# Kernel optimization log

Hardware: AMD Instinct MI355X
Metric: run time of the kernel (lower is better)

The kernel has to match this reference:

```python
import jax, jax.numpy as jnp
import numpy as np

_DN = ('NCHW', 'OIHW', 'NCHW')


def _gaussian_kernel1d(ksize, sigma):
    x = np.arange(ksize, dtype=np.float32) - ksize // 2
    g = np.exp(-x ** 2 / (2.0 * sigma ** 2))
    return (g / g.sum()).astype(np.float32)


def _nms_kernels():
    # kornia get_canny_nms_kernel: kernel k = center - neighbor at angle k*45deg (0deg = +x/right)
    k = np.zeros((8, 1, 3, 3), dtype=np.float32)
    offs = [(0, 1), (-1, 1), (-1, 0), (-1, -1), (0, -1), (1, -1), (1, 0), (1, 1)]
    for i, (dy, dx) in enumerate(offs):
        k[i, 0, 1, 1] = 1.0
        k[i, 0, 1 + dy, 1 + dx] = -1.0
    return k


def _conv(x, w, padding):
    return jax.lax.conv_general_dilated(x, w, (1, 1), padding, dimension_numbers=_DN)


def _canny_magnitude(data):
    eps = 1e-6
    x = (data + 1.0) / 2.0
    # rgb -> grayscale (kornia weights)
    rgb_w = jnp.array([0.299, 0.587, 0.114], dtype=x.dtype)
    gray = jnp.einsum('bchw,c->bhw', x, rgb_w)[:, None]  # [B,1,H,W]
    # gaussian blur 5x5, sigma=1, reflect border (kornia default), separable
    g1d = jnp.asarray(_gaussian_kernel1d(5, 1.0), dtype=x.dtype)
    p = jnp.pad(gray, ((0, 0), (0, 0), (2, 2), (2, 2)), mode='reflect')
    blurred = _conv(_conv(p, g1d.reshape(1, 1, 1, 5), 'VALID'), g1d.reshape(1, 1, 5, 1), 'VALID')
    # sobel spatial gradient (normalized=False), replicate padding
    sob_x = jnp.array([[-1., 0., 1.], [-2., 0., 2.], [-1., 0., 1.]], dtype=x.dtype)
    sob = jnp.stack([sob_x, sob_x.T])[:, None]  # [2,1,3,3]
    bp = jnp.pad(blurred, ((0, 0), (0, 0), (1, 1), (1, 1)), mode='edge')
    grads = _conv(bp, sob, 'VALID')  # [B,2,H,W]
    gx, gy = grads[:, 0:1], grads[:, 1:2]
    magnitude = jnp.sqrt(gx * gx + gy * gy + eps)  # [B,1,H,W]
    # angle rounded to nearest 45 degrees
    ang45 = jnp.round(jnp.rad2deg(jnp.arctan2(gy, gx)) / 45.0)
    # non-maximum suppression: center-minus-neighbor along 8 directions (zero pad)
    nms_k = jnp.asarray(_nms_kernels(), dtype=x.dtype)
    nms_mag = _conv(magnitude, nms_k, ((1, 1), (1, 1)))  # [B,8,H,W]
    idx_pos = ang45.astype(jnp.int32) % 8
    idx_neg = (idx_pos + 4) % 8
    sel_pos = jnp.take_along_axis(nms_mag, idx_pos, axis=1)
    sel_neg = jnp.take_along_axis(nms_mag, idx_neg, axis=1)
    is_max = jnp.minimum(sel_pos, sel_neg) > 0.0
    return magnitude * is_max


def setup_inputs() -> dict:
    key = jax.random.key(0)
    data = jax.random.normal(key, (16, 3, 512, 512), dtype=jnp.float32)
    return {'data': data}


def reference(data):
    # EdgeOperator.forward: canny((data+1)/2)[0] -> NMS'd gradient magnitude [B,1,H,W]
    return _canny_magnitude(data)
```

## Files before the change

kernel.cpp:

```cpp
#include <hip/hip_runtime.h>
#include <math.h>

#define IMH 512
#define IMW 512
#define RB    16
#define NBAND 32
#define NWC   10
#define OUTW  56

__device__ __forceinline__ int reflect_i(int v, int n) {
    if (v < 0) v = -v;
    if (v >= n) v = 2 * n - 2 - v;
    return v;
}
__device__ __forceinline__ float dpp_shr1(float x) {
    int i = __float_as_int(x);
    return __int_as_float(__builtin_amdgcn_update_dpp(i, i, 0x138, 0xF, 0xF, false));
}
__device__ __forceinline__ float dpp_shl1(float x) {
    int i = __float_as_int(x);
    return __int_as_float(__builtin_amdgcn_update_dpp(i, i, 0x130, 0xF, 0xF, false));
}

template <bool YB>
__device__ __forceinline__ void run_band(const float* __restrict__ p0,
                                         const float* __restrict__ p1,
                                         const float* __restrict__ p2,
                                         float* __restrict__ outp,
                                         int y0, int rx, int cx,
                                         int ixm, int ixp, int lane) {
    const float w0 = 0.05448868f, w1 = 0.24420134f, w2 = 0.40261995f;

    float h0 = 0, h1 = 0, h2 = 0, h3 = 0;
    float b_1 = 0, b_0 = 0, bl_1 = 0, bl_0 = 0, br_1 = 0, br_0 = 0;
    float m_1 = 0, m_0 = 0, ml_1 = 0, ml_0 = 0, mr_1 = 0, mr_0 = 0;
    float gxp = 0, gyp = 0;

    auto process = [&](int yL, float gray) {
        float gm1 = dpp_shr1(gray);
        float gm2 = dpp_shr1(gm1);
        float gp1 = dpp_shl1(gray);
        float gp2 = dpp_shl1(gp1);
        float hnew = w0 * (gm2 + gp2) + w1 * (gm1 + gp1) + w2 * gray;
        float bnew = w0 * (h0 + hnew) + w1 * (h1 + h3) + w2 * h2;
        float blnew = __shfl(bnew, ixm);
        float brnew = __shfl(bnew, ixp);
        int u = yL - 3;
        float ta  = (YB && u == 0) ? b_0 : b_1;
        float tla = (YB && u == 0) ? bl_0 : bl_1;
        float tra = (YB && u == 0) ? br_0 : br_1;
        float tb  = (YB && u == IMH - 1) ? b_0 : bnew;
        float tlb = (YB && u == IMH - 1) ? bl_0 : blnew;
        float trb = (YB && u == IMH - 1) ? br_0 : brnew;
        float gx = (tra - tla) + 2.0f * (br_0 - bl_0) + (trb - tlb);
        float gy = (tlb - tla) + 2.0f * (tb - ta) + (trb - tra);
        float mnew = sqrtf(gx * gx + gy * gy + 1e-6f);
        if ((unsigned)cx >= (unsigned)IMW) mnew = 0.0f;
        float mlnew = dpp_shr1(mnew);
        float mrnew = dpp_shl1(mnew);
        int s = yL - 4;
        if (s >= y0) {
            float pm  = (YB && s == 0) ? 0.0f : m_1;
            float pml = (YB && s == 0) ? 0.0f : ml_1;
            float pmr = (YB && s == 0) ? 0.0f : mr_1;
            float nm  = (YB && s == IMH - 1) ? 0.0f : mnew;
            float nml = (YB && s == IMH - 1) ? 0.0f : mlnew;
            float nmr = (YB && s == IMH - 1) ? 0.0f : mrnew;
            float ax = fabsf(gxp), ay = fabsf(gyp);
            bool ew = (ay <= 0.41421356237f * ax);
            bool ns = (ay >= 2.41421356237f * ax);
            bool d1 = (gxp * gyp > 0.0f);
            float n1 = ew ? mr_0 : (ns ? nm : (d1 ? pmr : nmr));
            float n2 = ew ? ml_0 : (ns ? pm : (d1 ? nml : pml));
            float mag = m_0;
            float o = (mag > n1 && mag > n2) ? mag : 0.0f;
            if (lane >= 4 && lane < 60 && (unsigned)cx < (unsigned)IMW)
                __builtin_nontemporal_store(o, &outp[(size_t)s * IMW + cx]);
        }
        h0 = h1; h1 = h2; h2 = h3; h3 = hnew;
        b_1 = b_0;  b_0 = bnew;
        bl_1 = bl_0; bl_0 = blnew;
        br_1 = br_0; br_0 = brnew;
        m_1 = m_0;  m_0 = mnew;
        ml_1 = ml_0; ml_0 = mlnew;
        mr_1 = mr_0; mr_0 = mrnew;
        gxp = gx; gyp = gy;
    };

    int ya = reflect_i(y0 - 4, IMH) * IMW;
    float rA = p0[ya + rx], gA = p1[ya + rx], cA = p2[ya + rx];
    int yb = reflect_i(y0 - 3, IMH) * IMW;
    float rB = p0[yb + rx], gB = p1[yb + rx], cB = p2[yb + rx];

    #pragma unroll 2
    for (int tt = 0; tt < (RB + 8) / 2; ++tt) {
        int yL = y0 - 4 + 2 * tt;
        float grayA = 0.1495f * rA + 0.2935f * gA + 0.057f * cA + 0.5f;
        int yr = reflect_i(yL + 2, IMH) * IMW;
        rA = p0[yr + rx]; gA = p1[yr + rx]; cA = p2[yr + rx];
        process(yL, grayA);
        float grayB = 0.1495f * rB + 0.2935f * gB + 0.057f * cB + 0.5f;
        int yr2 = reflect_i(yL + 3, IMH) * IMW;
        rB = p0[yr2 + rx]; gB = p1[yr2 + rx]; cB = p2[yr2 + rx];
        process(yL + 1, grayB);
    }
}

__global__ __launch_bounds__(256)
void canny_stream(const float* __restrict__ data, float* __restrict__ out) {
    const int lane = threadIdx.x & 63;
    const int wid  = (blockIdx.x << 2) + (threadIdx.x >> 6);
    const int wc   = wid % NWC;
    const int t2   = wid / NWC;
    const int band = t2 & (NBAND - 1);
    const int bat  = t2 >> 5;

    const int c0 = OUTW * wc - 4;
    const int cx = c0 + lane;
    const int y0 = band * RB;

    const size_t plane = (size_t)(IMH * IMW);
    const float* p0 = data + (size_t)bat * 3 * plane;
    const float* p1 = p0 + plane;
    const float* p2 = p1 + plane;
    float* outp = out + (size_t)bat * plane;

    const int rx  = reflect_i(cx, IMW);
    const int ixm = (cx - 1 < 0 ? 0 : (cx - 1 >= IMW ? IMW - 1 : cx - 1)) - c0;
    const int ixp = (cx + 1 < 0 ? 0 : (cx + 1 >= IMW ? IMW - 1 : cx + 1)) - c0;

    if (band == 0 || band == NBAND - 1)
        run_band<true>(p0, p1, p2, outp, y0, rx, cx, ixm, ixp, lane);
    else
        run_band<false>(p0, p1, p2, outp, y0, rx, cx, ixm, ixp, lane);
}

extern "C" void kernel_launch(void* const* d_in, const int* in_sizes, int n_in,
                              void* d_out, int out_size, void* d_ws, size_t ws_size,
                              hipStream_t stream) {
    const float* data = (const float*)d_in[0];
    float* out = (float*)d_out;
    int B = in_sizes[0] / (3 * IMH * IMW);
    int blocks = (B * NBAND * NWC) / 4;
    canny_stream<<<blocks, dim3(256, 1, 1), 0, stream>>>(data, out);
}
```

Baseline: 93.21 us.

## Process two columns per lane with float2 loads and x-border specialization

Each lane now handles two adjacent columns, so a wave covers 128 columns with a 4-column halo on each side instead of 64 with a 4-column halo. This cuts redundant halo loads and compute, and halves the number of waves (NWC 10→5). Loads and stores become float2/64-bit vectors, and the __shfl neighbour exchanges are replaced by DPP shifts. A new XB template splits border tiles from interior ones so interior tiles skip column reflection and validity checks. The cost is higher register pressure and fewer waves in flight, which lowers occupancy and latency hiding.

After: 98.03 us. 5.2% more time.

```diff
diff --git a/kernel.cpp b/kernel.cpp
--- a/kernel.cpp
+++ b/kernel.cpp
@@ -5,8 +5,8 @@
 #define IMW 512
 #define RB    16
 #define NBAND 32
-#define NWC   10
-#define OUTW  56
+#define NWC   5
+#define OUTW  120
 
 __device__ __forceinline__ int reflect_i(int v, int n) {
     if (v < 0) v = -v;
@@ -22,87 +22,133 @@
     return __int_as_float(__builtin_amdgcn_update_dpp(i, i, 0x130, 0xF, 0xF, false));
 }
 
-template <bool YB>
+template <bool YB, bool XB>
 __device__ __forceinline__ void run_band(const float* __restrict__ p0,
                                          const float* __restrict__ p1,
                                          const float* __restrict__ p2,
                                          float* __restrict__ outp,
-                                         int y0, int rx, int cx,
-                                         int ixm, int ixp, int lane) {
+                                         int y0, int c0, int lane) {
     const float w0 = 0.05448868f, w1 = 0.24420134f, w2 = 0.40261995f;
+    const int cx0 = c0 + 2 * lane, cx1 = cx0 + 1;
+    int rx0 = 0, rx1 = 0;
+    bool vx0 = true, vx1 = true;
+    if (XB) {
+        rx0 = reflect_i(cx0, IMW); rx1 = reflect_i(cx1, IMW);
+        vx0 = (unsigned)cx0 < (unsigned)IMW;
+        vx1 = (unsigned)cx1 < (unsigned)IMW;
+    }
+    const bool storeok = (lane >= 2) && (lane <= 61) &&
+                         (!XB || (unsigned)cx0 < (unsigned)IMW);
 
-    float h0 = 0, h1 = 0, h2 = 0, h3 = 0;
-    float b_1 = 0, b_0 = 0, bl_1 = 0, bl_0 = 0, br_1 = 0, br_0 = 0;
-    float m_1 = 0, m_0 = 0, ml_1 = 0, ml_0 = 0, mr_1 = 0, mr_0 = 0;
-    float gxp = 0, gyp = 0;
+    float hA0 = 0, hA1 = 0, hA2 = 0, hA3 = 0, hB0 = 0, hB1 = 0, hB2 = 0, hB3 = 0;
+    float bp0_1 = 0, bp1_1 = 0, bp0_0 = 0, bp1_0 = 0;
+    float bl_1 = 0, bl_0 = 0, br_1 = 0, br_0 = 0;
+    float mp0_1 = 0, mp1_1 = 0, mp0_0 = 0, mp1_0 = 0;
+    float ml_1 = 0, ml_0 = 0, mr_1 = 0, mr_0 = 0;
+    float gxp0 = 0, gxp1 = 0, gyp0 = 0, gyp1 = 0;
 
-    auto process = [&](int yL, float gray) {
-        float gm1 = dpp_shr1(gray);
-        float gm2 = dpp_shr1(gm1);
-        float gp1 = dpp_shl1(gray);
-        float gp2 = dpp_shl1(gp1);
-        float hnew = w0 * (gm2 + gp2) + w1 * (gm1 + gp1) + w2 * gray;
-        float bnew = w0 * (h0 + hnew) + w1 * (h1 + h3) + w2 * h2;
-        float blnew = __shfl(bnew, ixm);
-        float brnew = __shfl(bnew, ixp);
+    auto loadrow = [&](int y, float2& R, float2& G, float2& Bc) {
+        int yy = YB ? reflect_i(y, IMH) : y;
+        int yo = yy * IMW;
+        if (XB) {
+            R.x = p0[yo + rx0]; R.y = p0[yo + rx1];
+            G.x = p1[yo + rx0]; G.y = p1[yo + rx1];
+            Bc.x = p2[yo + rx0]; Bc.y = p2[yo + rx1];
+        } else {
+            R  = *(const float2*)(p0 + yo + cx0);
+            G  = *(const float2*)(p1 + yo + cx0);
+            Bc = *(const float2*)(p2 + yo + cx0);
+        }
+    };
+    auto grayf = [&](const float2& R, const float2& G, const float2& Bc) {
+        float2 g;
+        g.x = 0.1495f * R.x + 0.2935f * G.x + 0.057f * Bc.x;
+        g.y = 0.1495f * R.y + 0.2935f * G.y + 0.057f * Bc.y;
+        return g;
+    };
+
+    auto process = [&](int yL, float2 Gp) {
+        float g1L = dpp_shr1(Gp.y);
+        float g0L = dpp_shr1(Gp.x);
+        float g0R = dpp_shl1(Gp.x);
+        float g1R = dpp_shl1(Gp.y);
+        float h0n = w0 * (g0L + g0R) + w1 * (g1L + Gp.y) + w2 * Gp.x;
+        float h1n = w0 * (g1L + g1R) + w1 * (Gp.x + g0R) + w2 * Gp.y;
+        float b0n = w0 * (hA0 + h0n) + w1 * (hA1 + hA3) + w2 * hA2;
+        float b1n = w0 * (hB0 + h1n) + w1 * (hB1 + hB3) + w2 * hB2;
+        float bl1n = dpp_shr1(b1n);
+        float br0n = dpp_shl1(b0n);
+        if (XB) {
+            if (cx0 == 0)       bl1n = b0n;
+            if (cx1 == IMW - 1) br0n = b1n;
+        }
         int u = yL - 3;
-        float ta  = (YB && u == 0) ? b_0 : b_1;
-        float tla = (YB && u == 0) ? bl_0 : bl_1;
-        float tra = (YB && u == 0) ? br_0 : br_1;
-        float tb  = (YB && u == IMH - 1) ? b_0 : bnew;
-        float tlb = (YB && u == IMH - 1) ? bl_0 : blnew;
-        float trb = (YB && u == IMH - 1) ? br_0 : brnew;
-        float gx = (tra - tla) + 2.0f * (br_0 - bl_0) + (trb - tlb);
-        float gy = (tlb - tla) + 2.0f * (tb - ta) + (trb - tra);
-        float mnew = sqrtf(gx * gx + gy * gy + 1e-6f);
-        if ((unsigned)cx >= (unsigned)IMW) mnew = 0.0f;
-        float mlnew = dpp_shr1(mnew);
-        float mrnew = dpp_shl1(mnew);
+        float t_b0 = bp0_1, t_b1 = bp1_1, t_bl = bl_1, t_br = br_1;
+        float n_b0 = b0n,   n_b1 = b1n,   n_bl = bl1n, n_br = br0n;
+        if (YB) {
+            if (u == 0)       { t_b0 = bp0_0; t_b1 = bp1_0; t_bl = bl_0; t_br = br_0; }
+            if (u == IMH - 1) { n_b0 = bp0_0; n_b1 = bp1_0; n_bl = bl_0; n_br = br_0; }
+        }
+        float gx0 = (t_b1 - t_bl) + 2.0f * (bp1_0 - bl_0) + (n_b1 - n_bl);
+        float gy0 = (n_bl - t_bl) + 2.0f * (n_b0 - t_b0) + (n_b1 - t_b1);
+        float gx1 = (t_br - t_b0) + 2.0f * (br_0 - bp0_0) + (n_br - n_b0);
+        float gy1 = (n_b0 - t_b0) + 2.0f * (n_b1 - t_b1) + (n_br - t_br);
+        float mg0 = __builtin_amdgcn_sqrtf(gx0 * gx0 + gy0 * gy0 + 1e-6f);
+        float mg1 = __builtin_amdgcn_sqrtf(gx1 * gx1 + gy1 * gy1 + 1e-6f);
+        if (XB) { if (!vx0) mg0 = 0.0f; if (!vx1) mg1 = 0.0f; }
+        float mln = dpp_shr1(mg1);
+        float mrn = dpp_shl1(mg0);
         int s = yL - 4;
         if (s >= y0) {
-            float pm  = (YB && s == 0) ? 0.0f : m_1;
-            float pml = (YB && s == 0) ? 0.0f : ml_1;
-            float pmr = (YB && s == 0) ? 0.0f : mr_1;
-            float nm  = (YB && s == IMH - 1) ? 0.0f : mnew;
-            float nml = (YB && s == IMH - 1) ? 0.0f : mlnew;
-            float nmr = (YB && s == IMH - 1) ? 0.0f : mrnew;
-            float ax = fabsf(gxp), ay = fabsf(gyp);
-            bool ew = (ay <= 0.41421356237f * ax);
-            bool ns = (ay >= 2.41421356237f * ax);
-            bool d1 = (gxp * gyp > 0.0f);
-            float n1 = ew ? mr_0 : (ns ? nm : (d1 ? pmr : nmr));
-            float n2 = ew ? ml_0 : (ns ? pm : (d1 ? nml : pml));
-            float mag = m_0;
-            float o = (mag > n1 && mag > n2) ? mag : 0.0f;
-            if (lane >= 4 && lane < 60 && (unsigned)cx < (unsigned)IMW)
-                __builtin_nontemporal_store(o, &outp[(size_t)s * IMW + cx]);
+            float pm0 = mp0_1, pm1 = mp1_1, pml = ml_1, pmr = mr_1;
+            float nm0 = mg0,   nm1 = mg1,   nml = mln,  nmr = mrn;
+            if (YB) {
+                if (s == 0)       { pm0 = 0; pm1 = 0; pml = 0; pmr = 0; }
+                if (s == IMH - 1) { nm0 = 0; nm1 = 0; nml = 0; nmr = 0; }
+            }
+            float ax0 = fabsf(gxp0), ay0 = fabsf(gyp0);
+            bool ew0 = ay0 <= 0.41421356237f * ax0;
+            bool ns0 = ay0 >= 2.41421356237f * ax0;
+            bool d10 = gxp0 * gyp0 > 0.0f;
+            float n1a = ew0 ? mp1_0 : (ns0 ? nm0 : (d10 ? pm1 : nm1));
+            float n2a = ew0 ? ml_0  : (ns0 ? pm0 : (d10 ? nml : pml));
+            float o0 = (mp0_0 > n1a && mp0_0 > n2a) ? mp0_0 : 0.0f;
+            float ax1 = fabsf(gxp1), ay1 = fabsf(gyp1);
+            bool ew1 = ay1 <= 0.41421356237f * ax1;
+            bool ns1 = ay1 >= 2.41421356237f * ax1;
+            bool d11 = gxp1 * gyp1 > 0.0f;
+            float n1b = ew1 ? mr_0  : (ns1 ? nm1 : (d11 ? pmr : nmr));
+            float n2b = ew1 ? mp0_0 : (ns1 ? pm1 : (d11 ? nm0 : pm0));
+            float o1 = (mp1_0 > n1b && mp1_0 > n2b) ? mp1_0 : 0.0f;
+            if (storeok) {
+                union { float f[2]; unsigned long long u; } pk;
+                pk.f[0] = o0; pk.f[1] = o1;
+                __builtin_nontemporal_store(
+                    pk.u, (unsigned long long*)(outp + (size_t)s * IMW + cx0));
+            }
         }
-        h0 = h1; h1 = h2; h2 = h3; h3 = hnew;
-        b_1 = b_0;  b_0 = bnew;
-        bl_1 = bl_0; bl_0 = blnew;
-        br_1 = br_0; br_0 = brnew;
-        m_1 = m_0;  m_0 = mnew;
-        ml_1 = ml_0; ml_0 = mlnew;
-        mr_1 = mr_0; mr_0 = mrnew;
-        gxp = gx; gyp = gy;
+        hA0 = hA1; hA1 = hA2; hA2 = hA3; hA3 = h0n;
+        hB0 = hB1; hB1 = hB2; hB2 = hB3; hB3 = h1n;
+        bp0_1 = bp0_0; bp0_0 = b0n;  bp1_1 = bp1_0; bp1_0 = b1n;
+        bl_1 = bl_0; bl_0 = bl1n;    br_1 = br_0; br_0 = br0n;
+        mp0_1 = mp0_0; mp0_0 = mg0;  mp1_1 = mp1_0; mp1_0 = mg1;
+        ml_1 = ml_0; ml_0 = mln;     mr_1 = mr_0; mr_0 = mrn;
+        gxp0 = gx0; gxp1 = gx1; gyp0 = gy0; gyp1 = gy1;
     };
 
-    int ya = reflect_i(y0 - 4, IMH) * IMW;
-    float rA = p0[ya + rx], gA = p1[ya + rx], cA = p2[ya + rx];
-    int yb = reflect_i(y0 - 3, IMH) * IMW;
-    float rB = p0[yb + rx], gB = p1[yb + rx], cB = p2[yb + rx];
+    float2 rA, gA, cA, rB, gB, cB;
+    loadrow(y0 - 4, rA, gA, cA);
+    loadrow(y0 - 3, rB, gB, cB);
 
     #pragma unroll 2
     for (int tt = 0; tt < (RB + 8) / 2; ++tt) {
         int yL = y0 - 4 + 2 * tt;
-        float grayA = 0.1495f * rA + 0.2935f * gA + 0.057f * cA + 0.5f;
-        int yr = reflect_i(yL + 2, IMH) * IMW;
-        rA = p0[yr + rx]; gA = p1[yr + rx]; cA = p2[yr + rx];
-        process(yL, grayA);
-        float grayB = 0.1495f * rB + 0.2935f * gB + 0.057f * cB + 0.5f;
-        int yr2 = reflect_i(yL + 3, IMH) * IMW;
-        rB = p0[yr2 + rx]; gB = p1[yr2 + rx]; cB = p2[yr2 + rx];
-        process(yL + 1, grayB);
+        float2 GA = grayf(rA, gA, cA);
+        loadrow(yL + 2, rA, gA, cA);
+        process(yL, GA);
+        float2 GB = grayf(rB, gB, cB);
+        loadrow(yL + 3, rB, gB, cB);
+        process(yL + 1, GB);
     }
 }
 
@@ -116,7 +162,6 @@
     const int bat  = t2 >> 5;
 
     const int c0 = OUTW * wc - 4;
-    const int cx = c0 + lane;
     const int y0 = band * RB;
 
     const size_t plane = (size_t)(IMH * IMW);
@@ -125,14 +170,15 @@
     const float* p2 = p1 + plane;
     float* outp = out + (size_t)bat * plane;
 
-    const int rx  = reflect_i(cx, IMW);
-    const int ixm = (cx - 1 < 0 ? 0 : (cx - 1 >= IMW ? IMW - 1 : cx - 1)) - c0;
-    const int ixp = (cx + 1 < 0 ? 0 : (cx + 1 >= IMW ? IMW - 1 : cx + 1)) - c0;
-
-    if (band == 0 || band == NBAND - 1)
-        run_band<true>(p0, p1, p2, outp, y0, rx, cx, ixm, ixp, lane);
-    else
-        run_band<false>(p0, p1, p2, outp, y0, rx, cx, ixm, ixp, lane);
+    const bool yb = (band == 0) || (band == NBAND - 1);
+    const bool xb = (wc == 0) || (wc == NWC - 1);
+    if (yb) {
+        if (xb) run_band<true, true >(p0, p1, p2, outp, y0, c0, lane);
+        else    run_band<true, false>(p0, p1, p2, outp, y0, c0, lane);
+    } else {
+        if (xb) run_band<false, true >(p0, p1, p2, outp, y0, c0, lane);
+        else    run_band<false, false>(p0, p1, p2, outp, y0, c0, lane);
+    }
 }
 
 extern "C" void kernel_launch(void* const* d_in, const int* in_sizes, int n_in,
```
